# Optimization experiments

Measured on AMD Instinct MI355X. Metric: run time of the kernel, lower is better.

The kernel has to match this reference:

```python
import jax, jax.numpy as jnp
import numpy as np

IN_FEATURES = 4096
OUT_FEATURES = 11008
BATCH = 64


def setup_inputs() -> dict:
    key = jax.random.key(0)
    k_x, k_w, k_s, k_b = jax.random.split(key, 4)
    x = jax.random.normal(k_x, (BATCH, IN_FEATURES), dtype=jnp.float32)
    # int8-range quantized weights stored as int8 (symmetric, [-128, 127])
    weight_q = jax.random.randint(k_w, (OUT_FEATURES, IN_FEATURES), -128, 128, dtype=jnp.int8)
    # per-output-row scales, strictly positive (absmax/127 style)
    scale = jax.random.uniform(k_s, (OUT_FEATURES, 1), dtype=jnp.float32, minval=1e-4, maxval=2e-2)
    bias = jax.random.normal(k_b, (OUT_FEATURES,), dtype=jnp.float32)
    return {"x": x, "weight_q": weight_q, "scale": scale, "bias": bias}


def reference(x, weight_q, scale, bias):
    # on-the-fly dequantization: w_deq[o, i] = weight_q[o, i] * scale[o]
    w_deq = weight_q.astype(x.dtype) * scale.astype(x.dtype)  # [O, I]
    # F.linear: y = x @ w_deq.T + bias
    return jnp.einsum('bi,oi->bo', x, w_deq) + bias
```

## Files before the change

### kernel.cpp

```cpp
#include <hip/hip_runtime.h>

#define IN_F 4096
#define OUT_F 11008
#define BATCH 64
#define KSPLIT 8
#define STEPS (IN_F / 64 / KSPLIT)

typedef int v4i __attribute__((ext_vector_type(4)));
typedef signed char i8;

__device__ __forceinline__ int pack4(int a0, int a1, int a2, int a3) {
    return (a0 & 0xff) | ((a1 & 0xff) << 8) | ((a2 & 0xff) << 16) |
           ((unsigned)a3 << 24);
}

__global__ __launch_bounds__(256)
void quant_x_kernel(const float* __restrict__ x, i8* __restrict__ xq,
                    float* __restrict__ xscale)
{
    const int b = blockIdx.x;
    const int t = threadIdx.x;
    const float* xr = x + (size_t)b * IN_F;
    const int i0 = t * 16;

    float vals[16];
    float m = 0.0f;
#pragma unroll
    for (int j = 0; j < 16; ++j) {
        vals[j] = xr[i0 + j];
        m = fmaxf(m, fabsf(vals[j]));
    }

    __shared__ float red[256];
    red[t] = m;
    __syncthreads();
    for (int s = 128; s > 0; s >>= 1) {
        if (t < s) red[t] = fmaxf(red[t], red[t + s]);
        __syncthreads();
    }
    const float amax = red[0];
    const float inv = (amax > 0.0f) ? (127.0f / amax) : 0.0f;
    if (t == 0) xscale[b] = (amax > 0.0f) ? (amax / 127.0f) : 1.0f;

    const int kc   = i0 >> 6;
    const int quad = (i0 >> 4) & 3;
    const int mt   = b >> 4;
    const int lane = (b & 15) | (quad << 4);

    i8 q[16];
#pragma unroll
    for (int j = 0; j < 16; ++j) {
        float r = rintf(vals[j] * inv);
        r = fminf(127.0f, fmaxf(-127.0f, r));
        q[j] = (i8)(int)r;
    }
    v4i* dst = (v4i*)(xq + ((size_t)(kc * 256 + mt * 64 + lane) * 16));
    *dst = *(const v4i*)q;
}

__global__ __launch_bounds__(256)
void init_out_kernel(const float* __restrict__ bias, float* __restrict__ out)
{
    const int o = blockIdx.x * 256 + threadIdx.x;
    const int b = blockIdx.y;
    out[(size_t)b * OUT_F + o] = bias[o];
}

__global__ __launch_bounds__(256)
void gemm_kernel(const int* __restrict__ wq, const i8* __restrict__ xq,
                 const float* __restrict__ xscale,
                 const float* __restrict__ wscale,
                 float* __restrict__ out)
{
    const int lane  = threadIdx.x & 63;
    const int wave  = threadIdx.x >> 6;
    const int laneN = lane & 15;
    const int quad  = lane >> 4;

    const int n0  = blockIdx.x * 128;
    const int kc0 = blockIdx.y * STEPS;

    const int oA = n0 + wave * 32 + laneN;
    const int oB = oA + 16;

    const int kbase = kc0 * 64 + quad * 16;
    const int* pWA = wq + (size_t)oA * IN_F + kbase;
    const int* pWB = wq + (size_t)oB * IN_F + kbase;
    const v4i* pA  = (const v4i*)xq + (size_t)kc0 * 256 + lane;

    v4i acc[4][2];
#pragma unroll
    for (int mt = 0; mt < 4; ++mt)
#pragma unroll
        for (int nt = 0; nt < 2; ++nt)
            acc[mt][nt] = (v4i){0, 0, 0, 0};

    v4i rA[2][4];
    v4i aC[4], aN[4], bC[2];

#pragma unroll
    for (int r = 0; r < 4; ++r) {
        rA[0][r] = ((const v4i*)pWA)[r];
        rA[1][r] = ((const v4i*)pWB)[r];
    }
#pragma unroll
    for (int mt = 0; mt < 4; ++mt) aC[mt] = pA[mt * 64];
#pragma unroll
    for (int t = 0; t < 2; ++t)
        bC[t] = (v4i){pack4(rA[t][0][0], rA[t][0][1], rA[t][0][2], rA[t][0][3]),
                      pack4(rA[t][1][0], rA[t][1][1], rA[t][1][2], rA[t][1][3]),
                      pack4(rA[t][2][0], rA[t][2][1], rA[t][2][2], rA[t][2][3]),
                      pack4(rA[t][3][0], rA[t][3][1], rA[t][3][2], rA[t][3][3])};

#pragma unroll
    for (int s = 0; s < STEPS; ++s) {
        if (s + 1 < STEPS) {
            const v4i* nWA = (const v4i*)(pWA + (size_t)(s + 1) * 64);
            const v4i* nWB = (const v4i*)(pWB + (size_t)(s + 1) * 64);
#pragma unroll
            for (int r = 0; r < 4; ++r) {
                rA[0][r] = nWA[r];
                rA[1][r] = nWB[r];
            }
            const v4i* nA = pA + (size_t)(s + 1) * 256;
#pragma unroll
            for (int mt = 0; mt < 4; ++mt) aN[mt] = nA[mt * 64];
        }
#pragma unroll
        for (int mt = 0; mt < 4; ++mt) {
            acc[mt][0] = __builtin_amdgcn_mfma_i32_16x16x64_i8(aC[mt], bC[0], acc[mt][0], 0, 0, 0);
            acc[mt][1] = __builtin_amdgcn_mfma_i32_16x16x64_i8(aC[mt], bC[1], acc[mt][1], 0, 0, 0);
        }
        if (s + 1 < STEPS) {
#pragma unroll
            for (int t = 0; t < 2; ++t)
                bC[t] = (v4i){pack4(rA[t][0][0], rA[t][0][1], rA[t][0][2], rA[t][0][3]),
                              pack4(rA[t][1][0], rA[t][1][1], rA[t][1][2], rA[t][1][3]),
                              pack4(rA[t][2][0], rA[t][2][1], rA[t][2][2], rA[t][2][3]),
                              pack4(rA[t][3][0], rA[t][3][1], rA[t][3][2], rA[t][3][3])};
#pragma unroll
            for (int mt = 0; mt < 4; ++mt) aC[mt] = aN[mt];
        }
    }

    const float wsA = wscale[oA];
    const float wsB = wscale[oB];
    const int rbase = quad * 4;
#pragma unroll
    for (int mt = 0; mt < 4; ++mt) {
#pragma unroll
        for (int r = 0; r < 4; ++r) {
            const int brow = mt * 16 + rbase + r;
            const float xs = xscale[brow];
            atomicAdd(&out[(size_t)brow * OUT_F + oA], (float)acc[mt][0][r] * xs * wsA);
            atomicAdd(&out[(size_t)brow * OUT_F + oB], (float)acc[mt][1][r] * xs * wsB);
        }
    }
}

extern "C" void kernel_launch(void* const* d_in, const int* in_sizes, int n_in,
                              void* d_out, int out_size, void* d_ws, size_t ws_size,
                              hipStream_t stream)
{
    const float* x      = (const float*)d_in[0];
    const int*   wq     = (const int*)d_in[1];
    const float* wscale = (const float*)d_in[2];
    const float* bias   = (const float*)d_in[3];
    float* out = (float*)d_out;

    i8*    xq     = (i8*)d_ws;
    float* xscale = (float*)((char*)d_ws + (size_t)BATCH * IN_F);

    quant_x_kernel<<<BATCH, 256, 0, stream>>>(x, xq, xscale);
    init_out_kernel<<<dim3(OUT_F / 256, BATCH), 256, 0, stream>>>(bias, out);
    gemm_kernel<<<dim3(OUT_F / 128, KSPLIT), 256, 0, stream>>>(wq, xq, xscale, wscale, out);
}
```

Before: 269.6 us.

## Pre-pack weights into MFMA layout and replace atomics with split-K partial reduction

Adds a per-call pack kernel that reads the int32-stored weights, narrows them to int8 and transposes them through LDS into the MFMA operand layout. The GEMM can then load one coalesced 16-byte vector per lane with no packing arithmetic in its inner loop. Split-K results go to per-slice partial buffers instead of float atomics into the output. A separate vectorized reduce kernel sums the slices and adds the bias. The cost is an extra pass over the full weight matrix plus partial-buffer writes and reads each call, in exchange for removing the atomics and the in-loop repacking.

```diff
diff --git a/kernel.cpp b/kernel.cpp
--- a/kernel.cpp
+++ b/kernel.cpp
@@ -3,11 +3,19 @@
 #define IN_F 4096
 #define OUT_F 11008
 #define BATCH 64
-#define KSPLIT 8
-#define STEPS (IN_F / 64 / KSPLIT)
+#define NT (OUT_F / 16)
+#define NSTEP (IN_F / 64)
+#define KS 8
+#define SPW (NSTEP / KS)
 
 typedef int v4i __attribute__((ext_vector_type(4)));
+typedef float v4f __attribute__((ext_vector_type(4)));
 typedef signed char i8;
+
+#define WS_XQ 0u
+#define WS_XS (256u * 1024u)
+#define WS_WB (257u * 1024u)
+#define WS_PART (WS_WB + (size_t)OUT_F * IN_F)
 
 __device__ __forceinline__ int pack4(int a0, int a1, int a2, int a3) {
     return (a0 & 0xff) | ((a1 & 0xff) << 8) | ((a2 & 0xff) << 16) |
@@ -54,108 +62,105 @@
         r = fminf(127.0f, fmaxf(-127.0f, r));
         q[j] = (i8)(int)r;
     }
-    v4i* dst = (v4i*)(xq + ((size_t)(kc * 256 + mt * 64 + lane) * 16));
-    *dst = *(const v4i*)q;
+    *(v4i*)(xq + ((size_t)(kc * 256 + mt * 64 + lane) * 16)) = *(const v4i*)q;
 }
 
 __global__ __launch_bounds__(256)
-void init_out_kernel(const float* __restrict__ bias, float* __restrict__ out)
+void pack_w_kernel(const int* __restrict__ wq, i8* __restrict__ wb)
 {
-    const int o = blockIdx.x * 256 + threadIdx.x;
-    const int b = blockIdx.y;
-    out[(size_t)b * OUT_F + o] = bias[o];
+    const int nt = blockIdx.y;
+    const int sg = blockIdx.x;
+    const int t  = threadIdx.x;
+    const int row = t >> 4;
+    const int c   = t & 15;
+
+    __shared__ int lds[4 * 272];
+
+    const int* base = wq + (size_t)(nt * 16 + row) * IN_F + sg * 256 + c * 4;
+#pragma unroll
+    for (int r = 0; r < 4; ++r) {
+        v4i w = *(const v4i*)(base + r * 64);
+        lds[r * 272 + row * 17 + c] = pack4(w[0], w[1], w[2], w[3]);
+    }
+    __syncthreads();
+
+    const int sl = t >> 6;
+    const int L  = t & 63;
+    const int n  = t & 15;
+    const int q  = (t >> 4) & 3;
+    v4i o;
+#pragma unroll
+    for (int d = 0; d < 4; ++d)
+        o[d] = lds[sl * 272 + n * 17 + q * 4 + d];
+    *(v4i*)(wb + ((size_t)(nt * 64 + sg * 4 + sl) * 64 + L) * 16) = o;
 }
 
 __global__ __launch_bounds__(256)
-void gemm_kernel(const int* __restrict__ wq, const i8* __restrict__ xq,
+void gemm_kernel(const i8* __restrict__ wb, const i8* __restrict__ xq,
                  const float* __restrict__ xscale,
                  const float* __restrict__ wscale,
-                 float* __restrict__ out)
+                 float* __restrict__ part)
 {
-    const int lane  = threadIdx.x & 63;
-    const int wave  = threadIdx.x >> 6;
-    const int laneN = lane & 15;
-    const int quad  = lane >> 4;
+    const int lane = threadIdx.x & 63;
+    const int wave = threadIdx.x >> 6;
+    const int nt   = blockIdx.x * 4 + wave;
+    const int ks   = blockIdx.y;
 
-    const int n0  = blockIdx.x * 128;
-    const int kc0 = blockIdx.y * STEPS;
+    const v4i* pB = (const v4i*)wb + ((size_t)nt * 64 + ks * SPW) * 64 + lane;
+    const v4i* pA = (const v4i*)xq + (size_t)(ks * SPW) * 256 + lane;
 
-    const int oA = n0 + wave * 32 + laneN;
-    const int oB = oA + 16;
+    v4i acc[4];
+#pragma unroll
+    for (int mt = 0; mt < 4; ++mt) acc[mt] = (v4i){0, 0, 0, 0};
 
-    const int kbase = kc0 * 64 + quad * 16;
-    const int* pWA = wq + (size_t)oA * IN_F + kbase;
-    const int* pWB = wq + (size_t)oB * IN_F + kbase;
-    const v4i* pA  = (const v4i*)xq + (size_t)kc0 * 256 + lane;
-
-    v4i acc[4][2];
+    v4i bC, bN, aC[4], aN[4];
+    bC = pB[0];
 #pragma unroll
-    for (int mt = 0; mt < 4; ++mt)
-#pragma unroll
-        for (int nt = 0; nt < 2; ++nt)
-            acc[mt][nt] = (v4i){0, 0, 0, 0};
-
-    v4i rA[2][4];
-    v4i aC[4], aN[4], bC[2];
+    for (int mt = 0; mt < 4; ++mt) aC[mt] = pA[mt * 64];
 
 #pragma unroll
-    for (int r = 0; r < 4; ++r) {
-        rA[0][r] = ((const v4i*)pWA)[r];
-        rA[1][r] = ((const v4i*)pWB)[r];
-    }
+    for (int ss = 0; ss < SPW; ++ss) {
+        if (ss + 1 < SPW) {
+            bN = pB[(size_t)(ss + 1) * 64];
 #pragma unroll
-    for (int mt = 0; mt < 4; ++mt) aC[mt] = pA[mt * 64];
-#pragma unroll
-    for (int t = 0; t < 2; ++t)
-        bC[t] = (v4i){pack4(rA[t][0][0], rA[t][0][1], rA[t][0][2], rA[t][0][3]),
-                      pack4(rA[t][1][0], rA[t][1][1], rA[t][1][2], rA[t][1][3]),
-                      pack4(rA[t][2][0], rA[t][2][1], rA[t][2][2], rA[t][2][3]),
-                      pack4(rA[t][3][0], rA[t][3][1], rA[t][3][2], rA[t][3][3])};
-
-#pragma unroll
-    for (int s = 0; s < STEPS; ++s) {
-        if (s + 1 < STEPS) {
-            const v4i* nWA = (const v4i*)(pWA + (size_t)(s + 1) * 64);
-            const v4i* nWB = (const v4i*)(pWB + (size_t)(s + 1) * 64);
-#pragma unroll
-            for (int r = 0; r < 4; ++r) {
-                rA[0][r] = nWA[r];
-                rA[1][r] = nWB[r];
-            }
-            const v4i* nA = pA + (size_t)(s + 1) * 256;
-#pragma unroll
-            for (int mt = 0; mt < 4; ++mt) aN[mt] = nA[mt * 64];
+            for (int mt = 0; mt < 4; ++mt) aN[mt] = pA[(size_t)(ss + 1) * 256 + mt * 64];
         }
 #pragma unroll
-        for (int mt = 0; mt < 4; ++mt) {
-            acc[mt][0] = __builtin_amdgcn_mfma_i32_16x16x64_i8(aC[mt], bC[0], acc[mt][0], 0, 0, 0);
-            acc[mt][1] = __builtin_amdgcn_mfma_i32_16x16x64_i8(aC[mt], bC[1], acc[mt][1], 0, 0, 0);
-        }
-        if (s + 1 < STEPS) {
-#pragma unroll
-            for (int t = 0; t < 2; ++t)
-                bC[t] = (v4i){pack4(rA[t][0][0], rA[t][0][1], rA[t][0][2], rA[t][0][3]),
-                              pack4(rA[t][1][0], rA[t][1][1], rA[t][1][2], rA[t][1][3]),
-                              pack4(rA[t][2][0], rA[t][2][1], rA[t][2][2], rA[t][2][3]),
-                              pack4(rA[t][3][0], rA[t][3][1], rA[t][3][2], rA[t][3][3])};
+        for (int mt = 0; mt < 4; ++mt)
+            acc[mt] = __builtin_amdgcn_mfma_i32_16x16x64_i8(aC[mt], bC, acc[mt], 0, 0, 0);
+        if (ss + 1 < SPW) {
+            bC = bN;
 #pragma unroll
             for (int mt = 0; mt < 4; ++mt) aC[mt] = aN[mt];
         }
     }
 
-    const float wsA = wscale[oA];
-    const float wsB = wscale[oB];
-    const int rbase = quad * 4;
+    const int n = lane & 15;
+    const int o = nt * 16 + n;
+    const float wsc = wscale[o];
+    const int rbase = (lane >> 4) * 4;
+    float* pp = part + (size_t)ks * BATCH * OUT_F + o;
 #pragma unroll
     for (int mt = 0; mt < 4; ++mt) {
 #pragma unroll
         for (int r = 0; r < 4; ++r) {
             const int brow = mt * 16 + rbase + r;
-            const float xs = xscale[brow];
-            atomicAdd(&out[(size_t)brow * OUT_F + oA], (float)acc[mt][0][r] * xs * wsA);
-            atomicAdd(&out[(size_t)brow * OUT_F + oB], (float)acc[mt][1][r] * xs * wsB);
+            pp[(size_t)brow * OUT_F] = (float)acc[mt][r] * xscale[brow] * wsc;
         }
     }
+}
+
+__global__ __launch_bounds__(256)
+void reduce_kernel(const float* __restrict__ part, const float* __restrict__ bias,
+                   float* __restrict__ out)
+{
+    const int i = (blockIdx.x * 256 + threadIdx.x) * 4;
+    const int o = i % OUT_F;
+    v4f s = *(const v4f*)(bias + o);
+#pragma unroll
+    for (int ks = 0; ks < KS; ++ks)
+        s += *(const v4f*)(part + (size_t)ks * BATCH * OUT_F + i);
+    *(v4f*)(out + i) = s;
 }
 
 extern "C" void kernel_launch(void* const* d_in, const int* in_sizes, int n_in,
@@ -168,10 +173,13 @@
     const float* bias   = (const float*)d_in[3];
     float* out = (float*)d_out;
 
-    i8*    xq     = (i8*)d_ws;
-    float* xscale = (float*)((char*)d_ws + (size_t)BATCH * IN_F);
+    i8*    xq     = (i8*)d_ws + WS_XQ;
+    float* xscale = (float*)((char*)d_ws + WS_XS);
+    i8*    wb     = (i8*)d_ws + WS_WB;
+    float* partials = (float*)((char*)d_ws + WS_PART);
 
     quant_x_kernel<<<BATCH, 256, 0, stream>>>(x, xq, xscale);
-    init_out_kernel<<<dim3(OUT_F / 256, BATCH), 256, 0, stream>>>(bias, out);
-    gemm_kernel<<<dim3(OUT_F / 128, KSPLIT), 256, 0, stream>>>(wq, xq, xscale, wscale, out);
+    pack_w_kernel<<<dim3(16, NT), 256, 0, stream>>>(wq, wb);
+    gemm_kernel<<<dim3(NT / 4, KS), 256, 0, stream>>>(wb, xq, xscale, wscale, partials);
+    reduce_kernel<<<(BATCH * OUT_F) / 1024, 256, 0, stream>>>(partials, bias, out);
 }
```

Result: slower. 275.9 us (+2.3%).
